# Kernel optimization log

Hardware: AMD Instinct MI355X
Metric: run time of the kernel (lower is better)

## Reference

```python
import jax, jax.numpy as jnp
import numpy as np

B, D, L = 4, 512, 4096
N1, N2 = 1167, 8921


def setup_inputs() -> dict:
    key = jax.random.key(0)
    k1, k2, k3, k4 = jax.random.split(key, 4)
    H = jax.random.normal(k1, (B, D, L), dtype=jnp.float32)
    Q1_w = jax.random.normal(k2, (N1, D), dtype=jnp.float32) * (1.0 / np.sqrt(D))
    Q2_w = jax.random.normal(k3, (N2, D), dtype=jnp.float32) * (1.0 / np.sqrt(D))
    Q12_w = jax.random.normal(k4, (N2, N1), dtype=jnp.float32) * (1.0 / np.sqrt(N1))
    return {"H": H, "Q1_w": Q1_w, "Q2_w": Q2_w, "Q12_w": Q12_w}


def reference(H, Q1_w, Q2_w, Q12_w):
    # H: [b, d, l]; Q1_w: [n1, d]; Q2_w: [n2, d]; Q12_w: [n2, n1]
    # Level-1 label attention
    E1 = jnp.einsum('nd,bdl->bnl', Q1_w, H)          # [b, n1, l]
    A1 = jax.nn.softmax(E1, axis=2)
    C1 = jnp.einsum('bnl,bdl->bnd', A1, H)           # [b, n1, d]
    # Project level-1 context to level-2 label space
    C1 = jnp.einsum('mn,bnd->bmd', Q12_w, C1)        # [b, n2, d]
    # Level-2 queries modulated by level-1 context (elementwise)
    Q2 = Q2_w[None, :, :] * C1                       # [b, n2, d]
    E2 = jnp.einsum('bmd,bdl->bml', Q2, H)           # [b, n2, l]
    A2 = jax.nn.softmax(E2, axis=2)
    C2 = jnp.einsum('bml,bdl->bmd', A2, H)           # [b, n2, d]
    return (C2, A2)
```

## Files before the change

kernel.cpp:

```cpp
#include <hip/hip_runtime.h>
#include <hip/hip_bf16.h>

typedef __bf16 bf16_t;
typedef __bf16 bf16x8 __attribute__((ext_vector_type(8)));
typedef __bf16 bf16x4 __attribute__((ext_vector_type(4)));
typedef float  f32x4  __attribute__((ext_vector_type(4)));

#define BM 128
#define BN 128
#define BK 64

#define SBAR() asm volatile("s_barrier" ::: "memory")

__global__ __launch_bounds__(256) void cast_transpose_H(
    const float* __restrict__ H, bf16_t* __restrict__ Hb,
    bf16_t* __restrict__ HTb, int D, int L) {
  __shared__ bf16_t tile[32][33];
  int b = blockIdx.z;
  int l0 = blockIdx.x * 32, d0 = blockIdx.y * 32;
  const float* Hp = H + (size_t)b * D * L;
  bf16_t* Hbp = Hb + (size_t)b * D * L;
  bf16_t* HTp = HTb + (size_t)b * L * D;
  int tx = threadIdx.x, ty = threadIdx.y;
#pragma unroll
  for (int r = 0; r < 4; r++) {
    int d = d0 + ty + r * 8;
    float v = Hp[(size_t)d * L + l0 + tx];
    bf16_t bv = (bf16_t)v;
    tile[ty + r * 8][tx] = bv;
    Hbp[(size_t)d * L + l0 + tx] = bv;
  }
  __syncthreads();
#pragma unroll
  for (int r = 0; r < 4; r++) {
    int l = l0 + ty + r * 8;
    HTp[(size_t)l * D + d0 + tx] = tile[tx][ty + r * 8];
  }
}

__global__ void cast_w_pad(const float* __restrict__ in, bf16_t* __restrict__ out,
                           int cols, int ldo) {
  int c = blockIdx.x * 256 + threadIdx.x;
  int r = blockIdx.y;
  if (c < ldo) {
    float v = (c < cols) ? in[(size_t)r * cols + c] : 0.0f;
    out[(size_t)r * ldo + c] = (bf16_t)v;
  }
}

__global__ void zero_rows(bf16_t* __restrict__ p, int r0, int nr, long sb, int L) {
  long i = (long)blockIdx.x * 256 + threadIdx.x;
  int b = blockIdx.y;
  long tot = (long)nr * L / 8;
  if (i < tot) {
    bf16x8 z = {};
    *(bf16x8*)(p + ((long)b * sb + r0) * L + i * 8) = z;
  }
}

__device__ inline bf16x8 cvt8(float4 a, float4 b) {
  bf16x8 o;
  o[0] = (bf16_t)a.x; o[1] = (bf16_t)a.y; o[2] = (bf16_t)a.z; o[3] = (bf16_t)a.w;
  o[4] = (bf16_t)b.x; o[5] = (bf16_t)b.y; o[6] = (bf16_t)b.z; o[7] = (bf16_t)b.w;
  return o;
}

__device__ inline void gload_lds16(const bf16_t* g, bf16_t* l) {
  __builtin_amdgcn_global_load_lds(
      (const __attribute__((address_space(1))) void*)g,
      (__attribute__((address_space(3))) void*)l, 16, 0, 0);
}

__device__ inline void stage_half(const bf16_t* __restrict__ src, int ld,
                                  bf16_t* lds_half, int t, int wid) {
  int r = t >> 3;
  int gsl = (t & 7) ^ (r & 7);
  const bf16_t* g = src + (size_t)r * ld + gsl * 8;
  gload_lds16(g, lds_half + wid * 512);
  gload_lds16(g + (size_t)64 * ld, lds_half + 4096 + wid * 512);
}

template <int EPI>
__global__ __launch_bounds__(512) void gemm256_bt(
    const bf16_t* __restrict__ A, long sAb, const bf16_t* __restrict__ BT, long sBb,
    void* __restrict__ Cv, long sCb, const float* __restrict__ W,
    int M, int N, int K, int lda, int ldb, int ldc) {
  __shared__ __align__(16) bf16_t As[2][256][64];
  __shared__ __align__(16) bf16_t Bs[2][256][64];
  int b = blockIdx.z;
  A += (size_t)b * sAb;
  BT += (size_t)b * sBb;

  int nx = gridDim.x, ny = gridDim.y;
  int nwg = nx * ny;
  int bid = blockIdx.x + nx * blockIdx.y;
  int qq = nwg >> 3, rr = nwg & 7;
  int xcd = bid & 7, lin = bid >> 3;
  int swz = (xcd < rr ? xcd * (qq + 1) : rr * (qq + 1) + (xcd - rr) * qq) + lin;
  int m0 = (swz / ny) * 256;
  int n0 = (swz % ny) * 256;

  int t = threadIdx.x;
  int lane = t & 63, wid = t >> 6;
  int l15 = lane & 15, q = lane >> 4;
  int wm = (wid >> 2) * 128;
  int wn = (wid & 3) * 64;
  int NT = K >> 6;

  f32x4 acc[8][4];
#pragma unroll
  for (int i = 0; i < 8; i++)
#pragma unroll
    for (int j = 0; j < 4; j++)
#pragma unroll
      for (int e = 0; e < 4; e++) acc[i][j][e] = 0.0f;

  stage_half(BT + (size_t)(n0 + 0) * ldb, ldb, &Bs[0][0][0], t, wid);
  stage_half(BT + (size_t)(n0 + 128) * ldb, ldb, &Bs[0][128][0], t, wid);
  stage_half(A + (size_t)(m0 + 0) * lda, lda, &As[0][0][0], t, wid);
  stage_half(A + (size_t)(m0 + 128) * lda, lda, &As[0][128][0], t, wid);
  stage_half(BT + (size_t)(n0 + 0) * ldb + 64, ldb, &Bs[1][0][0], t, wid);
  stage_half(BT + (size_t)(n0 + 128) * ldb + 64, ldb, &Bs[1][128][0], t, wid);
  asm volatile("s_waitcnt vmcnt(4)" ::: "memory");
  SBAR();

  bf16x8 af[4][2];
  bf16x8 bF[2][2][2];

  for (int kt = 0; kt < NT; ++kt) {
    int buf = kt & 1;
    const bf16_t* An = A + (size_t)m0 * lda + (size_t)(kt + 1) * 64;
    const bf16_t* Bn2 = BT + (size_t)n0 * ldb + (size_t)(kt + 2) * 64;

    auto readA = [&](int mh) {
#pragma unroll
      for (int i = 0; i < 4; i++) {
        const char* rowp = (const char*)&As[buf][wm + mh * 64 + i * 16 + l15][0];
#pragma unroll
        for (int ks = 0; ks < 2; ks++)
          af[i][ks] = *(const bf16x8*)(rowp + ((((ks * 4 + q) ^ (l15 & 7))) << 4));
      }
    };
    auto readB = [&](int ch) {
#pragma unroll
      for (int j = 0; j < 2; j++) {
        const char* rowp = (const char*)&Bs[buf][wn + ch * 32 + j * 16 + l15][0];
#pragma unroll
        for (int ks = 0; ks < 2; ks++)
          bF[ch][j][ks] = *(const bf16x8*)(rowp + ((((ks * 4 + q) ^ (l15 & 7))) << 4));
      }
    };
    auto mmaq = [&](int mh, int ch) {
      __builtin_amdgcn_s_setprio(1);
#pragma unroll
      for (int i = 0; i < 4; i++)
#pragma unroll
        for (int j = 0; j < 2; j++)
#pragma unroll
          for (int ks = 0; ks < 2; ks++)
            acc[mh * 4 + i][ch * 2 + j] = __builtin_amdgcn_mfma_f32_16x16x32_bf16(
                af[i][ks], bF[ch][j][ks], acc[mh * 4 + i][ch * 2 + j], 0, 0, 0);
      __builtin_amdgcn_s_setprio(0);
    };

    readA(0);
    readB(0);
    if (kt + 1 < NT) stage_half(An, lda, &As[buf ^ 1][0][0], t, wid);
    SBAR();
    mmaq(0, 0);
    SBAR();
    readB(1);
    if (kt + 1 < NT) stage_half(An + (size_t)128 * lda, lda, &As[buf ^ 1][128][0], t, wid);
    SBAR();
    mmaq(0, 1);
    SBAR();
    readA(1);
    if (kt + 2 < NT) stage_half(Bn2, ldb, &Bs[buf][0][0], t, wid);
    SBAR();
    mmaq(1, 0);
    SBAR();
    if (kt + 2 < NT) {
      stage_half(Bn2 + (size_t)128 * ldb, ldb, &Bs[buf][128][0], t, wid);
      asm volatile("s_waitcnt vmcnt(4)" ::: "memory");
    } else if (kt + 1 < NT) {
      asm volatile("s_waitcnt vmcnt(0)" ::: "memory");
    }
    SBAR();
    mmaq(1, 1);
    SBAR();
  }

  float* sc = (float*)&As[0][0][0];
  float* Cp = (float*)Cv + (size_t)b * sCb;
#pragma unroll
  for (int ck = 0; ck < 4; ck++) {
    __syncthreads();
    if ((wid >> 2) == (ck >> 1)) {
      int igb = (ck & 1) * 4;
#pragma unroll
      for (int ii = 0; ii < 4; ii++) {
        int ig = igb + ii;
        int rl = ii * 16 + q * 4;
#pragma unroll
        for (int jg = 0; jg < 4; jg++) {
          int c = wn + jg * 16 + l15;
#pragma unroll
          for (int r4 = 0; r4 < 4; r4++)
            sc[(rl + r4) * 256 + c] = acc[ig][jg][r4];
        }
      }
    }
    __syncthreads();
    int rbase0 = m0 + ck * 64;
#pragma unroll
    for (int i = 0; i < 8; i++) {
      int idx = i * 512 + t;
      int r = idx >> 6;
      int c4 = idx & 63;
      int gr = rbase0 + r;
      if (gr < M) {
        f32x4 v = *(const f32x4*)(sc + idx * 4);
        __builtin_nontemporal_store(v, (f32x4*)(Cp + (size_t)gr * ldc) + (n0 >> 2) + c4);
      }
    }
  }
}

template <typename AT, int EPI>
__global__ __launch_bounds__(256) void gemm_bt(
    const AT* __restrict__ A, long sAb, const bf16_t* __restrict__ BT, long sBb,
    void* __restrict__ Cv, long sCb, const float* __restrict__ W,
    int M, int N, int K, int lda, int ldb, int ldc) {
  constexpr bool AF32 = (sizeof(AT) == 4);
  __shared__ __align__(16) bf16_t As[BM][BK];
  __shared__ __align__(16) bf16_t Bs[BN][BK];
  int b = blockIdx.z;
  A += (size_t)b * sAb;
  BT += (size_t)b * sBb;

  int nx = gridDim.x, ny = gridDim.y;
  int nwg = nx * ny;
  int bid = blockIdx.x + nx * blockIdx.y;
  int qq = nwg >> 3, rr = nwg & 7;
  int xcd = bid & 7, lin = bid >> 3;
  int swz = (xcd < rr ? xcd * (qq + 1) : rr * (qq + 1) + (xcd - rr) * qq) + lin;
  int m0 = (swz / ny) * BM;
  int n0 = (swz % ny) * BN;

  int t = threadIdx.x;
  int lane = t & 63, wid = t >> 6;
  int l15 = lane & 15, q = lane >> 4;
  int wm = (wid >> 1) * 64, wn = (wid & 1) * 64;

  int r0 = t >> 3;
  int sl = t & 7;
  int gsl = sl ^ (r0 & 7);
  bf16_t* lA = &As[0][0] + (size_t)wid * 512;
  bf16_t* lB = &Bs[0][0] + (size_t)wid * 512;

  f32x4 acc[4][4];
#pragma unroll
  for (int i = 0; i < 4; i++)
#pragma unroll
    for (int j = 0; j < 4; j++)
#pragma unroll
      for (int e = 0; e < 4; e++) acc[i][j][e] = 0.0f;

  for (int kb = 0; kb < K; kb += BK) {
    float4 va[4][2];
    if constexpr (AF32) {
#pragma unroll
      for (int i = 0; i < 4; i++) {
        int gm = m0 + i * 32 + r0;
        if (gm < M) {
          const float4* p = (const float4*)(A + (size_t)gm * lda + kb + gsl * 8);
          va[i][0] = p[0];
          va[i][1] = p[1];
        } else {
          va[i][0] = make_float4(0.f, 0.f, 0.f, 0.f);
          va[i][1] = make_float4(0.f, 0.f, 0.f, 0.f);
        }
      }
    }
    __syncthreads();
#pragma unroll
    for (int i = 0; i < 4; i++)
      gload_lds16(BT + (size_t)(n0 + i * 32 + r0) * ldb + kb + gsl * 8,
                  lB + i * 2048);
    if constexpr (AF32) {
#pragma unroll
      for (int i = 0; i < 4; i++)
        *(bf16x8*)(&As[0][0] + (size_t)(i * 256 + t) * 8) = cvt8(va[i][0], va[i][1]);
    } else {
#pragma unroll
      for (int i = 0; i < 4; i++)
        gload_lds16(A + (size_t)(m0 + i * 32 + r0) * lda + kb + gsl * 8,
                    lA + i * 2048);
    }
    __syncthreads();

#pragma unroll
    for (int ks = 0; ks < 2; ks++) {
      bf16x8 af[4], bfr[4];
#pragma unroll
      for (int i = 0; i < 4; i++) {
        int row = wm + i * 16 + l15;
        int off = (ks * 64 + q * 16) ^ ((l15 & 7) << 4);
        af[i] = *(const bf16x8*)((const char*)&As[row][0] + off);
      }
#pragma unroll
      for (int j = 0; j < 4; j++) {
        int row = wn + j * 16 + l15;
        int off = (ks * 64 + q * 16) ^ ((l15 & 7) << 4);
        bfr[j] = *(const bf16x8*)((const char*)&Bs[row][0] + off);
      }
#pragma unroll
      for (int i = 0; i < 4; i++)
#pragma unroll
        for (int j = 0; j < 4; j++)
          acc[i][j] = __builtin_amdgcn_mfma_f32_16x16x32_bf16(af[i], bfr[j],
                                                              acc[i][j], 0, 0, 0);
    }
  }

  if constexpr (EPI == 0) {
    float* sc = (float*)&As[0][0];
    float* Cp = (float*)Cv + (size_t)b * sCb;
#pragma unroll
    for (int ck = 0; ck < 4; ck++) {
      __syncthreads();
      if ((wid >> 1) == (ck >> 1)) {
        int ib = (ck & 1) * 2;
#pragma unroll
        for (int ii = 0; ii < 2; ii++) {
          int i = ib + ii;
          int rl = ii * 16 + q * 4;
#pragma unroll
          for (int j = 0; j < 4; j++) {
            int c = wn + j * 16 + l15;
#pragma unroll
            for (int r4 = 0; r4 < 4; r4++)
              sc[(rl + r4) * 128 + c] = acc[i][j][r4];
          }
        }
      }
      __syncthreads();
      int rbase0 = m0 + ck * 32;
#pragma unroll
      for (int i = 0; i < 4; i++) {
        int idx = i * 256 + t;
        int r = idx >> 5;
        int c4 = idx & 31;
        int gr = rbase0 + r;
        if (gr < M) {
          f32x4 v = *(const f32x4*)(sc + idx * 4);
          __builtin_nontemporal_store(v, (f32x4*)(Cp + (size_t)gr * ldc) + (n0 >> 2) + c4);
        }
      }
    }
  } else {
#pragma unroll
    for (int i = 0; i < 4; i++) {
      int rbase = m0 + wm + i * 16 + q * 4;
#pragma unroll
      for (int j = 0; j < 4; j++) {
        int c = n0 + wn + j * 16 + l15;
#pragma unroll
        for (int r4 = 0; r4 < 4; r4++) {
          int r = rbase + r4;
          if (r < M) {
            float val = acc[i][j][r4];
            if (EPI == 2) {
              float w = W[(size_t)r * N + c];
              bf16_t* Cp = (bf16_t*)Cv + (size_t)b * sCb;
              Cp[(size_t)r * ldc + c] = (bf16_t)(val * w);
            } else {
              bf16_t* Cp = (bf16_t*)Cv + (size_t)b * sCb;
              Cp[(size_t)r * ldc + c] = (bf16_t)val;
            }
          }
        }
      }
    }
  }
}

template <int MODE>
__global__ __launch_bounds__(256) void softmax_rows(
    const float* __restrict__ in, void* __restrict__ out,
    bf16_t* __restrict__ out2, int L, int ostr) {
  long row_in = (long)blockIdx.y * gridDim.x + blockIdx.x;
  long row_out = (long)blockIdx.y * ostr + blockIdx.x;
  const float* ip = in + row_in * L;
  int t = threadIdx.x;
  int lane = t & 63, wid = t >> 6;
  f32x4 v[4];
  float m = -3.4e38f;
#pragma unroll
  for (int c = 0; c < 4; c++) {
    if (MODE == 2)
      v[c] = __builtin_nontemporal_load((const f32x4*)ip + c * 256 + t);
    else
      v[c] = ((const f32x4*)ip)[c * 256 + t];
    m = fmaxf(m, fmaxf(fmaxf(v[c][0], v[c][1]), fmaxf(v[c][2], v[c][3])));
  }
#pragma unroll
  for (int off = 1; off < 64; off <<= 1) m = fmaxf(m, __shfl_xor(m, off));
  __shared__ float redm[4];
  __shared__ float reds[4];
  if (lane == 0) redm[wid] = m;
  __syncthreads();
  m = fmaxf(fmaxf(redm[0], redm[1]), fmaxf(redm[2], redm[3]));
  float s = 0.0f;
#pragma unroll
  for (int c = 0; c < 4; c++) {
    v[c][0] = __expf(v[c][0] - m);
    v[c][1] = __expf(v[c][1] - m);
    v[c][2] = __expf(v[c][2] - m);
    v[c][3] = __expf(v[c][3] - m);
    s += (v[c][0] + v[c][1]) + (v[c][2] + v[c][3]);
  }
#pragma unroll
  for (int off = 1; off < 64; off <<= 1) s += __shfl_xor(s, off);
  if (lane == 0) reds[wid] = s;
  __syncthreads();
  s = (reds[0] + reds[1]) + (reds[2] + reds[3]);
  float inv = 1.0f / s;
  if (MODE == 1) {
    bf16_t* op = (bf16_t*)out + row_out * L;
#pragma unroll
    for (int c = 0; c < 4; c++) {
      bf16x4 o;
      o[0] = (bf16_t)(v[c][0] * inv);
      o[1] = (bf16_t)(v[c][1] * inv);
      o[2] = (bf16_t)(v[c][2] * inv);
      o[3] = (bf16_t)(v[c][3] * inv);
      *(bf16x4*)(op + ((size_t)c * 256 + t) * 4) = o;
    }
  } else {
    float* op = (float*)out + row_out * L;
#pragma unroll
    for (int c = 0; c < 4; c++) {
      f32x4 o = v[c] * inv;
      if (MODE == 2) {
        __builtin_nontemporal_store(o, (f32x4*)op + c * 256 + t);
        bf16x4 ob;
        ob[0] = (bf16_t)o[0]; ob[1] = (bf16_t)o[1];
        ob[2] = (bf16_t)o[2]; ob[3] = (bf16_t)o[3];
        __builtin_nontemporal_store(ob, (bf16x4*)(out2 + row_out * L) + c * 256 + t);
      } else {
        ((f32x4*)op)[c * 256 + t] = o;
      }
    }
  }
}

extern "C" void kernel_launch(void* const* d_in, const int* in_sizes, int n_in,
                              void* d_out, int out_size, void* d_ws, size_t ws_size,
                              hipStream_t stream) {
  const int B = 4, D = 512, L = 4096, N1 = 1167, N2 = 8921;
  const int N1P = 1280;
  const int N1K = 1216;
  const int M2P = 8960;
  const float* H = (const float*)d_in[0];
  const float* Q1w = (const float*)d_in[1];
  const float* Q2w = (const float*)d_in[2];
  const float* Q12w = (const float*)d_in[3];
  float* C2 = (float*)d_out;
  float* A2 = C2 + (size_t)B * N2 * D;

  char* ws = (char*)d_ws;
  size_t off = 0;
  auto alloc = [&](size_t bytes) -> void* {
    void* p = ws + off;
    off = (off + bytes + 255) & ~(size_t)255;
    return p;
  };
  bf16_t* Hb   = (bf16_t*)alloc((size_t)B * D * L * 2);
  bf16_t* HTb  = (bf16_t*)alloc((size_t)B * L * D * 2);
  bf16_t* Q1b  = (bf16_t*)alloc((size_t)N1P * D * 2);
  bf16_t* Q12b = (bf16_t*)alloc((size_t)M2P * N1P * 2);
  float*  E1   = (float*)alloc((size_t)B * N1 * L * 4);
  bf16_t* A1b  = (bf16_t*)alloc((size_t)B * N1P * L * 2);
  bf16_t* C1Tb = (bf16_t*)alloc((size_t)B * D * N1P * 2);
  bf16_t* Q2b  = (bf16_t*)alloc(((size_t)B * N2 + 64) * D * 2);
  size_t a2b_bytes = ((size_t)B * N2 + 128) * (size_t)L * 2;
  bool useA2b = (ws_size > 0) && (off + a2b_bytes <= ws_size);
  bf16_t* A2b = (bf16_t*)alloc(a2b_bytes);

  cast_transpose_H<<<dim3(L / 32, D / 32, B), dim3(32, 8), 0, stream>>>(H, Hb, HTb, D, L);
  cast_w_pad<<<dim3((D + 255) / 256, N1), 256, 0, stream>>>(Q1w, Q1b, D, D);
  zero_rows<<<dim3(((N1P - N1) * D / 8 + 255) / 256, 1), 256, 0, stream>>>(
      Q1b, N1, N1P - N1, 0, D);
  cast_w_pad<<<dim3((N1P + 255) / 256, N2), 256, 0, stream>>>(Q12w, Q12b, N1, N1P);
  zero_rows<<<dim3(((N1P - N1) * L / 8 + 255) / 256, B), 256, 0, stream>>>(
      A1b, N1, N1P - N1, (long)N1P, L);
  gemm_bt<bf16_t, 0><<<dim3(N1P / BM, L / BN, B), 256, 0, stream>>>(
      Q1b, 0, HTb, (long)L * D, E1, (long)N1 * L, nullptr, N1, L, D, D, D, L);
  softmax_rows<1><<<dim3(N1, B), 256, 0, stream>>>(E1, A1b, nullptr, L, N1P);
  gemm_bt<bf16_t, 3><<<dim3(D / BM, N1P / BN, B), 256, 0, stream>>>(
      Hb, (long)D * L, A1b, (long)N1P * L, C1Tb, (long)D * N1P, nullptr,
      D, N1P, L, L, L, N1P);
  gemm_bt<bf16_t, 2><<<dim3(M2P / BM, D / BN, B), 256, 0, stream>>>(
      Q12b, 0, C1Tb, (long)D * N1P, Q2b, (long)N2 * D, Q2w, N2, D, N1K, N1P, N1P, D);
  gemm256_bt<0><<<dim3(M2P / 256, L / 256, B), 512, 0, stream>>>(
      Q2b, (long)N2 * D, HTb, (long)L * D, A2, (long)N2 * L, nullptr, N2, L, D, D, D, L);
  if (useA2b) {
    softmax_rows<2><<<dim3(B * N2, 1), 256, 0, stream>>>(A2, A2, A2b, L, 0);
    gemm_bt<bf16_t, 0><<<dim3(M2P / BM, D / BN, B), 256, 0, stream>>>(
        A2b, (long)N2 * L, Hb, (long)D * L, C2, (long)N2 * D, nullptr, N2, D, L, L, L, D);
  } else {
    softmax_rows<0><<<dim3(B * N2, 1), 256, 0, stream>>>(A2, A2, nullptr, L, 0);
    gemm_bt<float, 0><<<dim3(M2P / BM, D / BN, B), 256, 0, stream>>>(
        A2, (long)N2 * L, Hb, (long)D * L, C2, (long)N2 * D, nullptr, N2, D, L, L, L, D);
  }
}
```

Baseline: 1.604 ms.

## Split-K the level-1 context GEMM four ways with a separate reduction kernel

The A1·H GEMM that produces C1 previously ran with only a few hundred workgroups over a long K=4096 reduction. It now splits K into four slices along the grid z dimension, writes fp32 partial tiles to a workspace with regular stores, and sums them in a new reduce-and-cast kernel that emits the bf16 C1T buffer. This raises parallelism on the under-filled GEMM at the cost of extra partial-sum memory traffic and one more launch.

```diff
diff --git a/kernel.cpp b/kernel.cpp
--- a/kernel.cpp
+++ b/kernel.cpp
@@ -58,6 +58,24 @@
   }
 }
 
+__global__ void reduce4_bf16(const float* __restrict__ P, bf16_t* __restrict__ out,
+                             long slab) {
+  long i4 = (long)blockIdx.x * 256 + threadIdx.x;
+  int b = blockIdx.y;
+  if (i4 * 4 < slab) {
+    const float* p = P + (size_t)b * 4 * slab + i4 * 4;
+    f32x4 v0 = *(const f32x4*)(p);
+    f32x4 v1 = *(const f32x4*)(p + slab);
+    f32x4 v2 = *(const f32x4*)(p + 2 * slab);
+    f32x4 v3 = *(const f32x4*)(p + 3 * slab);
+    f32x4 s = (v0 + v1) + (v2 + v3);
+    bf16x4 o;
+    o[0] = (bf16_t)s[0]; o[1] = (bf16_t)s[1];
+    o[2] = (bf16_t)s[2]; o[3] = (bf16_t)s[3];
+    *(bf16x4*)(out + (size_t)b * slab + i4 * 4) = o;
+  }
+}
+
 __device__ inline bf16x8 cvt8(float4 a, float4 b) {
   bf16x8 o;
   o[0] = (bf16_t)a.x; o[1] = (bf16_t)a.y; o[2] = (bf16_t)a.z; o[3] = (bf16_t)a.w;
@@ -226,17 +244,19 @@
   }
 }
 
-template <typename AT, int EPI>
+template <typename AT, int EPI, bool NTS, int SPLITS>
 __global__ __launch_bounds__(256) void gemm_bt(
     const AT* __restrict__ A, long sAb, const bf16_t* __restrict__ BT, long sBb,
     void* __restrict__ Cv, long sCb, const float* __restrict__ W,
-    int M, int N, int K, int lda, int ldb, int ldc) {
+    int M, int N, int K, int lda, int ldb, int ldc, long sCs) {
   constexpr bool AF32 = (sizeof(AT) == 4);
   __shared__ __align__(16) bf16_t As[BM][BK];
   __shared__ __align__(16) bf16_t Bs[BN][BK];
-  int b = blockIdx.z;
-  A += (size_t)b * sAb;
-  BT += (size_t)b * sBb;
+  int zz = blockIdx.z;
+  int b = (SPLITS == 1) ? zz : zz / SPLITS;
+  int s = (SPLITS == 1) ? 0 : zz - b * SPLITS;
+  A += (size_t)b * sAb + (size_t)s * K;
+  BT += (size_t)b * sBb + (size_t)s * K;
 
   int nx = gridDim.x, ny = gridDim.y;
   int nwg = nx * ny;
@@ -325,7 +345,7 @@
 
   if constexpr (EPI == 0) {
     float* sc = (float*)&As[0][0];
-    float* Cp = (float*)Cv + (size_t)b * sCb;
+    float* Cp = (float*)Cv + (size_t)b * sCb + (size_t)s * sCs;
 #pragma unroll
     for (int ck = 0; ck < 4; ck++) {
       __syncthreads();
@@ -354,7 +374,9 @@
         int gr = rbase0 + r;
         if (gr < M) {
           f32x4 v = *(const f32x4*)(sc + idx * 4);
-          __builtin_nontemporal_store(v, (f32x4*)(Cp + (size_t)gr * ldc) + (n0 >> 2) + c4);
+          f32x4* dst = (f32x4*)(Cp + (size_t)gr * ldc) + (n0 >> 2) + c4;
+          if (NTS) __builtin_nontemporal_store(v, dst);
+          else *dst = v;
         }
       }
     }
@@ -462,6 +484,7 @@
   const int N1P = 1280;
   const int N1K = 1216;
   const int M2P = 8960;
+  const long SLAB5 = (long)D * N1P;
   const float* H = (const float*)d_in[0];
   const float* Q1w = (const float*)d_in[1];
   const float* Q2w = (const float*)d_in[2];
@@ -484,6 +507,7 @@
   bf16_t* A1b  = (bf16_t*)alloc((size_t)B * N1P * L * 2);
   bf16_t* C1Tb = (bf16_t*)alloc((size_t)B * D * N1P * 2);
   bf16_t* Q2b  = (bf16_t*)alloc(((size_t)B * N2 + 64) * D * 2);
+  float*  P5   = (float*)alloc((size_t)B * 4 * SLAB5 * 4);
   size_t a2b_bytes = ((size_t)B * N2 + 128) * (size_t)L * 2;
   bool useA2b = (ws_size > 0) && (off + a2b_bytes <= ws_size);
   bf16_t* A2b = (bf16_t*)alloc(a2b_bytes);
@@ -495,23 +519,24 @@
   cast_w_pad<<<dim3((N1P + 255) / 256, N2), 256, 0, stream>>>(Q12w, Q12b, N1, N1P);
   zero_rows<<<dim3(((N1P - N1) * L / 8 + 255) / 256, B), 256, 0, stream>>>(
       A1b, N1, N1P - N1, (long)N1P, L);
-  gemm_bt<bf16_t, 0><<<dim3(N1P / BM, L / BN, B), 256, 0, stream>>>(
-      Q1b, 0, HTb, (long)L * D, E1, (long)N1 * L, nullptr, N1, L, D, D, D, L);
+  gemm_bt<bf16_t, 0, true, 1><<<dim3(N1P / BM, L / BN, B), 256, 0, stream>>>(
+      Q1b, 0, HTb, (long)L * D, E1, (long)N1 * L, nullptr, N1, L, D, D, D, L, 0);
   softmax_rows<1><<<dim3(N1, B), 256, 0, stream>>>(E1, A1b, nullptr, L, N1P);
-  gemm_bt<bf16_t, 3><<<dim3(D / BM, N1P / BN, B), 256, 0, stream>>>(
-      Hb, (long)D * L, A1b, (long)N1P * L, C1Tb, (long)D * N1P, nullptr,
-      D, N1P, L, L, L, N1P);
-  gemm_bt<bf16_t, 2><<<dim3(M2P / BM, D / BN, B), 256, 0, stream>>>(
-      Q12b, 0, C1Tb, (long)D * N1P, Q2b, (long)N2 * D, Q2w, N2, D, N1K, N1P, N1P, D);
+  gemm_bt<bf16_t, 0, false, 4><<<dim3(D / BM, N1P / BN, B * 4), 256, 0, stream>>>(
+      Hb, (long)D * L, A1b, (long)N1P * L, P5, 4 * SLAB5, nullptr,
+      D, N1P, L / 4, L, L, N1P, SLAB5);
+  reduce4_bf16<<<dim3((SLAB5 / 4 + 255) / 256, B), 256, 0, stream>>>(P5, C1Tb, SLAB5);
+  gemm_bt<bf16_t, 2, true, 1><<<dim3(M2P / BM, D / BN, B), 256, 0, stream>>>(
+      Q12b, 0, C1Tb, (long)D * N1P, Q2b, (long)N2 * D, Q2w, N2, D, N1K, N1P, N1P, D, 0);
   gemm256_bt<0><<<dim3(M2P / 256, L / 256, B), 512, 0, stream>>>(
       Q2b, (long)N2 * D, HTb, (long)L * D, A2, (long)N2 * L, nullptr, N2, L, D, D, D, L);
   if (useA2b) {
     softmax_rows<2><<<dim3(B * N2, 1), 256, 0, stream>>>(A2, A2, A2b, L, 0);
-    gemm_bt<bf16_t, 0><<<dim3(M2P / BM, D / BN, B), 256, 0, stream>>>(
-        A2b, (long)N2 * L, Hb, (long)D * L, C2, (long)N2 * D, nullptr, N2, D, L, L, L, D);
+    gemm_bt<bf16_t, 0, true, 1><<<dim3(M2P / BM, D / BN, B), 256, 0, stream>>>(
+        A2b, (long)N2 * L, Hb, (long)D * L, C2, (long)N2 * D, nullptr, N2, D, L, L, L, D, 0);
   } else {
     softmax_rows<0><<<dim3(B * N2, 1), 256, 0, stream>>>(A2, A2, nullptr, L, 0);
-    gemm_bt<float, 0><<<dim3(M2P / BM, D / BN, B), 256, 0, stream>>>(
-        A2, (long)N2 * L, Hb, (long)D * L, C2, (long)N2 * D, nullptr, N2, D, L, L, L, D);
-  }
-}
+    gemm_bt<float, 0, true, 1><<<dim3(M2P / BM, D / BN, B), 256, 0, stream>>>(
+        A2, (long)N2 * L, Hb, (long)D * L, C2, (long)N2 * D, nullptr, N2, D, L, L, L, D, 0);
+  }
+}
```

New measurement: 1.591 ms. No clear change (-0.8%).
